# Kernel tuning notes

Measured on AMD Instinct MI355X. Metric: run time of the kernel, lower is better.

Reference implementation:

```python
import jax, jax.numpy as jnp
import numpy as np

MIN_NORM = 1e-15
BALL_EPS = 1e-3   # project() margin from ball boundary (c = 1)
TANH_CLIP = 15.0


def _norm(x):
    return jnp.sqrt(jnp.sum(x * x, axis=-1, keepdims=True)).clip(MIN_NORM)


def _tanh(x):
    return jnp.tanh(jnp.clip(x, -TANH_CLIP, TANH_CLIP))


def _artanh(x):
    return jnp.arctanh(jnp.clip(x, -1.0 + 1e-7, 1.0 - 1e-7))


def mobius_add(x, y):
    # Poincare ball Mobius addition, curvature c = 1
    x2 = jnp.sum(x * x, axis=-1, keepdims=True)
    y2 = jnp.sum(y * y, axis=-1, keepdims=True)
    xy = jnp.sum(x * y, axis=-1, keepdims=True)
    num = (1.0 + 2.0 * xy + y2) * x + (1.0 - x2) * y
    den = 1.0 + 2.0 * xy + x2 * y2
    return num / den.clip(MIN_NORM)


def project(x):
    norm = _norm(x)
    maxnorm = 1.0 - BALL_EPS
    return jnp.where(norm > maxnorm, x * (maxnorm / norm), x)


def expmap0(u):
    # exp map at the origin
    n = _norm(u)
    return _tanh(n) * u / n


def expmap(u, p):
    # exp map of tangent vector u at base point p
    n = _norm(u)
    p2 = jnp.sum(p * p, axis=-1, keepdims=True)
    lam = 2.0 / (1.0 - p2).clip(MIN_NORM)
    second = _tanh(0.5 * lam * n) * u / n
    return mobius_add(p, second)


def logmap(y, x):
    # log map of point y at base point x
    sub = mobius_add(-x, y)
    n = _norm(sub)
    x2 = jnp.sum(x * x, axis=-1, keepdims=True)
    lam = 2.0 / (1.0 - x2).clip(MIN_NORM)
    return (2.0 / lam) * _artanh(n) * sub / n


def setup_inputs() -> dict:
    key = jax.random.key(0)
    k1, k2, k3, k4 = jax.random.split(key, 4)
    n_entities, n_edges, n_rel, d = 100000, 800000, 32, 64
    # scale embeddings down so points stay well inside the unit ball
    ego_embed = 0.1 * jax.random.normal(k1, (n_entities, d), dtype=jnp.float32)
    relation_embed = 0.1 * jax.random.normal(k2, (n_rel, d), dtype=jnp.float32)
    edge_index = jax.random.randint(k3, (2, n_edges), 0, n_entities, dtype=jnp.int64)
    edge_type = jax.random.randint(k4, (n_edges,), 0, n_rel, dtype=jnp.int64)
    return {"ego_embed": ego_embed, "edge_index": edge_index,
            "edge_type": edge_type, "relation_embed": relation_embed}


def reference(ego_embed, edge_index, edge_type, relation_embed):
    head, tail = edge_index[0], edge_index[1]
    n_entities = ego_embed.shape[0]
    head_emb = ego_embed[head]          # [E, d] gather
    tail_emb = ego_embed[tail]          # [E, d] gather
    relation_emb = relation_embed[edge_type]  # [E, d] gather
    hyper_head = expmap0(head_emb)
    hyper_tail = expmap(tail_emb, hyper_head)
    hyper_rel = expmap(relation_emb, hyper_head)
    res = project(mobius_add(hyper_tail, hyper_rel))
    res = logmap(res, hyper_head)
    # scatter_mean over head index
    sums = jax.ops.segment_sum(res, head, num_segments=n_entities)
    counts = jax.ops.segment_sum(jnp.ones((head.shape[0],), dtype=res.dtype),
                                 head, num_segments=n_entities)
    entity_agg = sums / jnp.maximum(counts, 1.0)[:, None]
    return entity_agg
```

## Files before the change

### kernel.cpp

```cpp
#include <hip/hip_runtime.h>
#include <math.h>

#define D 64
#define MAXNORM 0.999f
#define MAXNORM2 (0.999f * 0.999f)
#define MIN_NORM 1e-15f
#define TANH_CLIP 15.0f
#define CAP 40

struct f4 { float x, y, z, w; };

__device__ __forceinline__ float frcp(float x) { return __builtin_amdgcn_rcpf(x); }
__device__ __forceinline__ float frsq(float x) { return __builtin_amdgcn_rsqf(x); }

__device__ __forceinline__ float dot8p(const f4& a0, const f4& a1,
                                       const f4& b0, const f4& b1) {
    return a0.x * b0.x + a0.y * b0.y + a0.z * b0.z + a0.w * b0.w +
           a1.x * b1.x + a1.y * b1.y + a1.z * b1.z + a1.w * b1.w;
}

__device__ __forceinline__ float rsum8(float v) {
    v += __shfl_xor(v, 1);
    v += __shfl_xor(v, 2);
    v += __shfl_xor(v, 4);
    return v;
}


__global__ void norm_kernel(const float* __restrict__ ego,
                            const float* __restrict__ rel,
                            float* __restrict__ norms,
                            float* __restrict__ relnorm,
                            float2* __restrict__ scal,
                            int N) {
    int wid = (blockIdx.x << 2) + (threadIdx.x >> 6);
    int lane = threadIdx.x & 63;
    if (wid >= N + 32) return;
    const float* src = (wid < N) ? (ego + (size_t)wid * D)
                                 : (rel + (size_t)(wid - N) * D);
    float v = src[lane];
    float s = v * v;
    s += __shfl_xor(s, 1);  s += __shfl_xor(s, 2);  s += __shfl_xor(s, 4);
    s += __shfl_xor(s, 8);  s += __shfl_xor(s, 16); s += __shfl_xor(s, 32);
    if (lane == 0) {
        float nh = sqrtf(s);
        if (wid < N) {
            norms[wid] = nh;
            float nhc = fmaxf(nh, MIN_NORM);
            float eh  = __expf(-2.0f * fminf(nhc, TANH_CLIP));
            float fp  = (1.0f - eh) * frcp((1.0f + eh) * nhc);
            float th2 = fp * fp * nhc * nhc;
            float tol = fmaxf(1.0f - th2, MIN_NORM);
            scal[wid] = make_float2(fp, tol);
        } else {
            relnorm[wid - N] = nh;
        }
    }
}


__global__ void bucket_kernel(const int* __restrict__ eidx,
                              const int* __restrict__ etype,
                              int* __restrict__ cnt,
                              int* __restrict__ bucket, int E) {
    int e = blockIdx.x * blockDim.x + threadIdx.x;
    if (e >= E) return;
    int head = eidx[e];
    int pos = atomicAdd(&cnt[head], 1);
    if (pos < CAP)
        bucket[head * CAP + pos] = eidx[E + e] | (etype[e] << 17);
}


__global__ void __launch_bounds__(256) agg_kernel(
        const float* __restrict__ ego,
        const float* __restrict__ rel,
        const int* __restrict__ cnt,
        const int* __restrict__ bucket,
        const float* __restrict__ norms,
        const float* __restrict__ relnorm,
        const float2* __restrict__ scal,
        float* __restrict__ out,
        int N) {
    int wid = (blockIdx.x * blockDim.x + threadIdx.x) >> 6;
    if (wid >= N) return;
    int lane = threadIdx.x & 63;
    int slot = lane >> 3;
    int sub  = lane & 7;

    int h = wid;
    const float* hrow = ego + (size_t)h * D;
    f4 h0 = *(const f4*)(hrow + sub * 4);
    f4 h1 = *(const f4*)(hrow + 32 + sub * 4);

    float2 sc2 = scal[h];
    float fp  = sc2.x;
    float tol = sc2.y;
    float p2  = 1.0f - tol;
    float hl  = frcp(tol);

    const int* brow = bucket + (size_t)h * CAP;
    int c = cnt[h];
    int cc = (c < CAP) ? c : CAP;
    f4 a0 = {0.f, 0.f, 0.f, 0.f}, a1 = {0.f, 0.f, 0.f, 0.f};
    float accP = 0.f;

    for (int i = slot; i < cc; i += 8) {
        int pk   = brow[i];
        int tail = pk & 0x1FFFF;
        int type = pk >> 17;

        const float* trow = ego + (size_t)tail * D;
        f4 t0 = *(const f4*)(trow + sub * 4);
        f4 t1 = *(const f4*)(trow + 32 + sub * 4);
        const float* rrow = rel + (size_t)type * D;
        f4 r0 = *(const f4*)(rrow + sub * 4);
        f4 r1 = *(const f4*)(rrow + 32 + sub * 4);
        float nt = norms[tail];
        float nr = relnorm[type];

        float d_ht = rsum8(dot8p(h0, h1, t0, t1));
        float d_hr = rsum8(dot8p(h0, h1, r0, r1));
        float d_tr = rsum8(dot8p(t0, t1, r0, r1));

        float t2 = nt * nt, r2 = nr * nr;
        float pt = fp * d_ht;
        float pr = fp * d_hr;

        float ntc = fmaxf(nt, MIN_NORM);
        float et  = __expf(-2.0f * fminf(hl * ntc, TANH_CLIP));
        float ft  = (1.0f - et) * frcp((1.0f + et) * ntc);
        float pyt = ft * pt;
        float yt2 = ft * ft * t2;
        float o1t = fmaf(2.0f, pyt, 1.0f);
        float at  = o1t + yt2;
        float invt = frcp(fmaf(p2, yt2, o1t));
        float At = at * invt;
        float Bt = tol * ft * invt;
        float x2 = (at - tol) * invt;

        float nrc = fmaxf(nr, MIN_NORM);
        float er  = __expf(-2.0f * fminf(hl * nrc, TANH_CLIP));
        float fr  = (1.0f - er) * frcp((1.0f + er) * nrc);
        float pyr = fr * pr;
        float gr  = fr * nr;
        float yr2 = gr * gr;
        float o1r = fmaf(2.0f, pyr, 1.0f);
        float ar  = o1r + yr2;
        float invr = frcp(fmaf(p2, yr2, o1r));
        float Ar = ar * invr;
        float Br = tol * fr * invr;
        float y2 = (ar - tol) * invr;

        float xy = At * Ar * p2 + At * Br * pr + Ar * Bt * pt + Bt * Br * d_tr;
        float o1m = fmaf(2.0f, xy, 1.0f);
        float am = o1m + y2;
        float bm = 1.0f - x2;
        float invm = frcp(fmaf(x2, y2, o1m));
        float al = (am * At + bm * Ar) * invm;
        float be = am * Bt * invm;
        float ga = bm * Br * invm;
        float m2 = fmaxf((am - bm) * invm, 1e-30f);

        if (m2 > MAXNORM2) {
            float s_ = MAXNORM * frsq(m2);
            al *= s_; be *= s_; ga *= s_;
            m2 = MAXNORM2;
        }

        float pm   = al * p2 + be * pt + ga * pr;
        float o2   = fmaf(-2.0f, pm, 1.0f);
        float invs = frcp(fmaf(p2, m2, o2));
        float om   = o2 + m2;
        float smm  = tol * invs;
        float u = fmaf(smm, al, -om * invs);
        float v = smm * be;
        float w = smm * ga;
        float s2 = fmaxf((om - tol) * invs, 1e-30f);

        float irs = frsq(s2);
        float ns  = fminf(s2 * irs, 1.0f - 1e-7f);
        float art = 0.5f * __logf((1.0f + ns) * frcp(1.0f - ns));
        float scv = tol * art * irs;

        float ct = scv * v, cr = scv * w;
        accP = fmaf(scv, u, accP);
        a0.x += ct * t0.x + cr * r0.x;  a0.y += ct * t0.y + cr * r0.y;
        a0.z += ct * t0.z + cr * r0.z;  a0.w += ct * t0.w + cr * r0.w;
        a1.x += ct * t1.x + cr * r1.x;  a1.y += ct * t1.y + cr * r1.y;
        a1.z += ct * t1.z + cr * r1.z;  a1.w += ct * t1.w + cr * r1.w;
    }

    #define RED(x) x += __shfl_xor(x, 8); x += __shfl_xor(x, 16); x += __shfl_xor(x, 32);
    RED(accP)
    RED(a0.x) RED(a0.y) RED(a0.z) RED(a0.w)
    RED(a1.x) RED(a1.y) RED(a1.z) RED(a1.w)
    #undef RED

    if (slot == 0) {
        float invc = frcp(fmaxf((float)c, 1.0f));
        float hp = accP * fp * invc;
        f4 o0, o1;
        o0.x = hp * h0.x + a0.x * invc;  o0.y = hp * h0.y + a0.y * invc;
        o0.z = hp * h0.z + a0.z * invc;  o0.w = hp * h0.w + a0.w * invc;
        o1.x = hp * h1.x + a1.x * invc;  o1.y = hp * h1.y + a1.y * invc;
        o1.z = hp * h1.z + a1.z * invc;  o1.w = hp * h1.w + a1.w * invc;
        float* orow = out + (size_t)h * D;
        *(f4*)(orow + sub * 4)      = o0;
        *(f4*)(orow + 32 + sub * 4) = o1;
    }
}

extern "C" void kernel_launch(void* const* d_in, const int* in_sizes, int n_in,
                              void* d_out, int out_size, void* d_ws, size_t ws_size,
                              hipStream_t stream) {
    const float* ego  = (const float*)d_in[0];
    const int*   eidx = (const int*)d_in[1];
    const int*   etyp = (const int*)d_in[2];
    const float* rel  = (const float*)d_in[3];
    float* out = (float*)d_out;

    int E = in_sizes[1] / 2;
    int N = in_sizes[0] / D;

    float2* scal  = (float2*)d_ws;
    int* cnt      = (int*)(scal + N);
    int* bucket   = cnt + N;
    float* norms   = (float*)(bucket + (size_t)N * CAP);
    float* relnorm = norms + N;

    hipMemsetAsync(cnt, 0, (size_t)N * sizeof(int), stream);

    const int tpb = 256;
    int eblocks = (E + tpb - 1) / tpb;
    int nblocks4 = (N + 32 + 3) / 4;

    norm_kernel<<<nblocks4, tpb, 0, stream>>>(ego, rel, norms, relnorm, scal, N);
    bucket_kernel<<<eblocks, tpb, 0, stream>>>(eidx, etyp, cnt, bucket, E);

    int nblocks = (N + 3) / 4;
    agg_kernel<<<nblocks, tpb, 0, stream>>>(ego, rel, cnt, bucket,
                                            norms, relnorm, scal, out, N);
}
```

Baseline: 158.4 us.

## Fuse norm and bucket kernels; widen edge parallelism to 16 slots per head

Merges the norm and bucket kernels into a single launch whose block range selects the role, removing one kernel launch and its serialization. In the aggregation kernel each wavefront now handles 16 edges at once with 4 lanes per edge, each lane owning 16 floats, instead of 8 edges with 8 lanes each. This halves the cross-lane shuffles needed for the dot products. The final reduction over slots now goes through shared memory instead of shuffles, so the kernel needs more registers for the accumulators and adds LDS traffic. Out-of-range wavefronts are clamped rather than exiting early so every thread reaches the shared-memory reduction.

```diff
diff --git a/kernel.cpp b/kernel.cpp
--- a/kernel.cpp
+++ b/kernel.cpp
@@ -13,27 +13,32 @@
 __device__ __forceinline__ float frcp(float x) { return __builtin_amdgcn_rcpf(x); }
 __device__ __forceinline__ float frsq(float x) { return __builtin_amdgcn_rsqf(x); }
 
-__device__ __forceinline__ float dot8p(const f4& a0, const f4& a1,
-                                       const f4& b0, const f4& b1) {
-    return a0.x * b0.x + a0.y * b0.y + a0.z * b0.z + a0.w * b0.w +
-           a1.x * b1.x + a1.y * b1.y + a1.z * b1.z + a1.w * b1.w;
-}
-
-__device__ __forceinline__ float rsum8(float v) {
-    v += __shfl_xor(v, 1);
-    v += __shfl_xor(v, 2);
-    v += __shfl_xor(v, 4);
-    return v;
-}
-
-
-__global__ void norm_kernel(const float* __restrict__ ego,
-                            const float* __restrict__ rel,
-                            float* __restrict__ norms,
-                            float* __restrict__ relnorm,
-                            float2* __restrict__ scal,
-                            int N) {
-    int wid = (blockIdx.x << 2) + (threadIdx.x >> 6);
+__device__ __forceinline__ float dot4(const f4& a, const f4& b) {
+    return a.x * b.x + a.y * b.y + a.z * b.z + a.w * b.w;
+}
+
+
+__global__ void setup_kernel(const float* __restrict__ ego,
+                             const float* __restrict__ rel,
+                             const int* __restrict__ eidx,
+                             const int* __restrict__ etype,
+                             int* __restrict__ cnt,
+                             int* __restrict__ bucket,
+                             float* __restrict__ norms,
+                             float* __restrict__ relnorm,
+                             float2* __restrict__ scal,
+                             int N, int E, int eblocks) {
+    if (blockIdx.x < eblocks) {
+        int e = blockIdx.x * 256 + threadIdx.x;
+        if (e < E) {
+            int head = eidx[e];
+            int pos = atomicAdd(&cnt[head], 1);
+            if (pos < CAP)
+                bucket[head * CAP + pos] = eidx[E + e] | (etype[e] << 17);
+        }
+        return;
+    }
+    int wid = (blockIdx.x - eblocks) * 4 + (threadIdx.x >> 6);
     int lane = threadIdx.x & 63;
     if (wid >= N + 32) return;
     const float* src = (wid < N) ? (ego + (size_t)wid * D)
@@ -59,19 +64,6 @@
 }
 
 
-__global__ void bucket_kernel(const int* __restrict__ eidx,
-                              const int* __restrict__ etype,
-                              int* __restrict__ cnt,
-                              int* __restrict__ bucket, int E) {
-    int e = blockIdx.x * blockDim.x + threadIdx.x;
-    if (e >= E) return;
-    int head = eidx[e];
-    int pos = atomicAdd(&cnt[head], 1);
-    if (pos < CAP)
-        bucket[head * CAP + pos] = eidx[E + e] | (etype[e] << 17);
-}
-
-
 __global__ void __launch_bounds__(256) agg_kernel(
         const float* __restrict__ ego,
         const float* __restrict__ rel,
@@ -82,16 +74,23 @@
         const float2* __restrict__ scal,
         float* __restrict__ out,
         int N) {
+    __shared__ float red[4][16][68];
+
     int wid = (blockIdx.x * blockDim.x + threadIdx.x) >> 6;
-    if (wid >= N) return;
+    int w    = threadIdx.x >> 6;
     int lane = threadIdx.x & 63;
-    int slot = lane >> 3;
-    int sub  = lane & 7;
-
-    int h = wid;
+    int slot = lane >> 2;
+    int sub  = lane & 3;
+
+    bool valid = (wid < N);
+    int h = valid ? wid : (N - 1);
+
     const float* hrow = ego + (size_t)h * D;
-    f4 h0 = *(const f4*)(hrow + sub * 4);
-    f4 h1 = *(const f4*)(hrow + 32 + sub * 4);
+    const float* hsub = hrow + sub * 16;
+    f4 h0 = *(const f4*)(hsub);
+    f4 h1 = *(const f4*)(hsub + 4);
+    f4 h2 = *(const f4*)(hsub + 8);
+    f4 h3 = *(const f4*)(hsub + 12);
 
     float2 sc2 = scal[h];
     float fp  = sc2.x;
@@ -102,28 +101,35 @@
     const int* brow = bucket + (size_t)h * CAP;
     int c = cnt[h];
     int cc = (c < CAP) ? c : CAP;
-    f4 a0 = {0.f, 0.f, 0.f, 0.f}, a1 = {0.f, 0.f, 0.f, 0.f};
+    f4 a0 = {0,0,0,0}, a1 = {0,0,0,0}, a2 = {0,0,0,0}, a3 = {0,0,0,0};
     float accP = 0.f;
 
-    for (int i = slot; i < cc; i += 8) {
+    for (int i = slot; i < cc; i += 16) {
         int pk   = brow[i];
         int tail = pk & 0x1FFFF;
         int type = pk >> 17;
 
-        const float* trow = ego + (size_t)tail * D;
-        f4 t0 = *(const f4*)(trow + sub * 4);
-        f4 t1 = *(const f4*)(trow + 32 + sub * 4);
-        const float* rrow = rel + (size_t)type * D;
-        f4 r0 = *(const f4*)(rrow + sub * 4);
-        f4 r1 = *(const f4*)(rrow + 32 + sub * 4);
+        const float* trow = ego + (size_t)tail * D + sub * 16;
+        f4 t0 = *(const f4*)(trow);
+        f4 t1 = *(const f4*)(trow + 4);
+        f4 t2 = *(const f4*)(trow + 8);
+        f4 t3 = *(const f4*)(trow + 12);
+        const float* rrow = rel + (size_t)type * D + sub * 16;
+        f4 r0 = *(const f4*)(rrow);
+        f4 r1 = *(const f4*)(rrow + 4);
+        f4 r2 = *(const f4*)(rrow + 8);
+        f4 r3 = *(const f4*)(rrow + 12);
         float nt = norms[tail];
         float nr = relnorm[type];
 
-        float d_ht = rsum8(dot8p(h0, h1, t0, t1));
-        float d_hr = rsum8(dot8p(h0, h1, r0, r1));
-        float d_tr = rsum8(dot8p(t0, t1, r0, r1));
-
-        float t2 = nt * nt, r2 = nr * nr;
+        float d_ht = dot4(h0,t0) + dot4(h1,t1) + dot4(h2,t2) + dot4(h3,t3);
+        float d_hr = dot4(h0,r0) + dot4(h1,r1) + dot4(h2,r2) + dot4(h3,r3);
+        float d_tr = dot4(t0,r0) + dot4(t1,r1) + dot4(t2,r2) + dot4(t3,r3);
+        d_ht += __shfl_xor(d_ht, 1); d_ht += __shfl_xor(d_ht, 2);
+        d_hr += __shfl_xor(d_hr, 1); d_hr += __shfl_xor(d_hr, 2);
+        d_tr += __shfl_xor(d_tr, 1); d_tr += __shfl_xor(d_tr, 2);
+
+        float t2n = nt * nt, r2n = nr * nr;
         float pt = fp * d_ht;
         float pr = fp * d_hr;
 
@@ -131,7 +137,7 @@
         float et  = __expf(-2.0f * fminf(hl * ntc, TANH_CLIP));
         float ft  = (1.0f - et) * frcp((1.0f + et) * ntc);
         float pyt = ft * pt;
-        float yt2 = ft * ft * t2;
+        float yt2 = ft * ft * t2n;
         float o1t = fmaf(2.0f, pyt, 1.0f);
         float at  = o1t + yt2;
         float invt = frcp(fmaf(p2, yt2, o1t));
@@ -175,7 +181,7 @@
         float smm  = tol * invs;
         float u = fmaf(smm, al, -om * invs);
         float v = smm * be;
-        float w = smm * ga;
+        float wv = smm * ga;
         float s2 = fmaxf((om - tol) * invs, 1e-30f);
 
         float irs = frsq(s2);
@@ -183,31 +189,43 @@
         float art = 0.5f * __logf((1.0f + ns) * frcp(1.0f - ns));
         float scv = tol * art * irs;
 
-        float ct = scv * v, cr = scv * w;
+        float ct = scv * v, cr = scv * wv;
         accP = fmaf(scv, u, accP);
-        a0.x += ct * t0.x + cr * r0.x;  a0.y += ct * t0.y + cr * r0.y;
-        a0.z += ct * t0.z + cr * r0.z;  a0.w += ct * t0.w + cr * r0.w;
-        a1.x += ct * t1.x + cr * r1.x;  a1.y += ct * t1.y + cr * r1.y;
-        a1.z += ct * t1.z + cr * r1.z;  a1.w += ct * t1.w + cr * r1.w;
-    }
-
-    #define RED(x) x += __shfl_xor(x, 8); x += __shfl_xor(x, 16); x += __shfl_xor(x, 32);
-    RED(accP)
-    RED(a0.x) RED(a0.y) RED(a0.z) RED(a0.w)
-    RED(a1.x) RED(a1.y) RED(a1.z) RED(a1.w)
-    #undef RED
-
-    if (slot == 0) {
+        a0.x = fmaf(ct, t0.x, fmaf(cr, r0.x, a0.x));
+        a0.y = fmaf(ct, t0.y, fmaf(cr, r0.y, a0.y));
+        a0.z = fmaf(ct, t0.z, fmaf(cr, r0.z, a0.z));
+        a0.w = fmaf(ct, t0.w, fmaf(cr, r0.w, a0.w));
+        a1.x = fmaf(ct, t1.x, fmaf(cr, r1.x, a1.x));
+        a1.y = fmaf(ct, t1.y, fmaf(cr, r1.y, a1.y));
+        a1.z = fmaf(ct, t1.z, fmaf(cr, r1.z, a1.z));
+        a1.w = fmaf(ct, t1.w, fmaf(cr, r1.w, a1.w));
+        a2.x = fmaf(ct, t2.x, fmaf(cr, r2.x, a2.x));
+        a2.y = fmaf(ct, t2.y, fmaf(cr, r2.y, a2.y));
+        a2.z = fmaf(ct, t2.z, fmaf(cr, r2.z, a2.z));
+        a2.w = fmaf(ct, t2.w, fmaf(cr, r2.w, a2.w));
+        a3.x = fmaf(ct, t3.x, fmaf(cr, r3.x, a3.x));
+        a3.y = fmaf(ct, t3.y, fmaf(cr, r3.y, a3.y));
+        a3.z = fmaf(ct, t3.z, fmaf(cr, r3.z, a3.z));
+        a3.w = fmaf(ct, t3.w, fmaf(cr, r3.w, a3.w));
+    }
+
+    accP += __shfl_xor(accP, 4);  accP += __shfl_xor(accP, 8);
+    accP += __shfl_xor(accP, 16); accP += __shfl_xor(accP, 32);
+
+    float* myrow = &red[w][slot][sub * 16];
+    *(f4*)(myrow)      = a0;
+    *(f4*)(myrow + 4)  = a1;
+    *(f4*)(myrow + 8)  = a2;
+    *(f4*)(myrow + 12) = a3;
+    float tot = 0.f;
+    #pragma unroll
+    for (int s = 0; s < 16; s++) tot += red[w][s][lane];
+
+    if (valid) {
         float invc = frcp(fmaxf((float)c, 1.0f));
         float hp = accP * fp * invc;
-        f4 o0, o1;
-        o0.x = hp * h0.x + a0.x * invc;  o0.y = hp * h0.y + a0.y * invc;
-        o0.z = hp * h0.z + a0.z * invc;  o0.w = hp * h0.w + a0.w * invc;
-        o1.x = hp * h1.x + a1.x * invc;  o1.y = hp * h1.y + a1.y * invc;
-        o1.z = hp * h1.z + a1.z * invc;  o1.w = hp * h1.w + a1.w * invc;
-        float* orow = out + (size_t)h * D;
-        *(f4*)(orow + sub * 4)      = o0;
-        *(f4*)(orow + 32 + sub * 4) = o1;
+        float hd = hrow[lane];
+        out[(size_t)h * D + lane] = fmaf(hp, hd, tot * invc);
     }
 }
 
@@ -233,10 +251,10 @@
 
     const int tpb = 256;
     int eblocks = (E + tpb - 1) / tpb;
-    int nblocks4 = (N + 32 + 3) / 4;
-
-    norm_kernel<<<nblocks4, tpb, 0, stream>>>(ego, rel, norms, relnorm, scal, N);
-    bucket_kernel<<<eblocks, tpb, 0, stream>>>(eidx, etyp, cnt, bucket, E);
+    int norm_blocks = (N + 32 + 3) / 4;
+
+    setup_kernel<<<eblocks + norm_blocks, tpb, 0, stream>>>(
+        ego, rel, eidx, etyp, cnt, bucket, norms, relnorm, scal, N, E, eblocks);
 
     int nblocks = (N + 3) / 4;
     agg_kernel<<<nblocks, tpb, 0, stream>>>(ego, rel, cnt, bucket,
```

Result: slower. 172.5 us (+8.9%).

## Sort heads by degree for aggregation and merge norm and bucket kernels

Applied to the files above, without the earlier changes.

Merges the norm and bucketing kernels into one launch, split by block index. Adds a degree histogram plus rank and order kernels that counting-sort heads by clamped degree, so each agg wavefront and block gets heads with similar edge counts. The aim is to cut loop-trip divergence and load imbalance in agg_kernel. In exchange it adds two kernel launches, hot atomics on a 41-bin histogram, and scattered head accesses and output writes.

```diff
diff --git a/kernel.cpp b/kernel.cpp
--- a/kernel.cpp
+++ b/kernel.cpp
@@ -7,6 +7,7 @@
 #define MIN_NORM 1e-15f
 #define TANH_CLIP 15.0f
 #define CAP 40
+#define NBIN 41
 
 struct f4 { float x, y, z, w; };
 
@@ -27,13 +28,27 @@
 }
 
 
-__global__ void norm_kernel(const float* __restrict__ ego,
-                            const float* __restrict__ rel,
-                            float* __restrict__ norms,
-                            float* __restrict__ relnorm,
-                            float2* __restrict__ scal,
-                            int N) {
-    int wid = (blockIdx.x << 2) + (threadIdx.x >> 6);
+__global__ void setup_kernel(const float* __restrict__ ego,
+                             const float* __restrict__ rel,
+                             const int* __restrict__ eidx,
+                             const int* __restrict__ etype,
+                             int* __restrict__ cnt,
+                             int* __restrict__ bucket,
+                             float* __restrict__ norms,
+                             float* __restrict__ relnorm,
+                             float2* __restrict__ scal,
+                             int N, int E, int eblocks) {
+    if (blockIdx.x < eblocks) {
+        int e = blockIdx.x * 256 + threadIdx.x;
+        if (e < E) {
+            int head = eidx[e];
+            int pos = atomicAdd(&cnt[head], 1);
+            if (pos < CAP)
+                bucket[head * CAP + pos] = eidx[E + e] | (etype[e] << 17);
+        }
+        return;
+    }
+    int wid = (blockIdx.x - eblocks) * 4 + (threadIdx.x >> 6);
     int lane = threadIdx.x & 63;
     if (wid >= N + 32) return;
     const float* src = (wid < N) ? (ego + (size_t)wid * D)
@@ -59,16 +74,31 @@
 }
 
 
-__global__ void bucket_kernel(const int* __restrict__ eidx,
-                              const int* __restrict__ etype,
-                              int* __restrict__ cnt,
-                              int* __restrict__ bucket, int E) {
-    int e = blockIdx.x * blockDim.x + threadIdx.x;
-    if (e >= E) return;
-    int head = eidx[e];
-    int pos = atomicAdd(&cnt[head], 1);
-    if (pos < CAP)
-        bucket[head * CAP + pos] = eidx[E + e] | (etype[e] << 17);
+__global__ void rank_kernel(const int* __restrict__ cnt,
+                            int* __restrict__ deghist,
+                            int* __restrict__ rankb, int N) {
+    int h = blockIdx.x * blockDim.x + threadIdx.x;
+    if (h >= N) return;
+    int d = cnt[h];
+    if (d > CAP) d = CAP;
+    rankb[h] = atomicAdd(&deghist[d], 1);
+}
+
+__global__ void order_kernel(const int* __restrict__ cnt,
+                             const int* __restrict__ deghist,
+                             const int* __restrict__ rankb,
+                             int* __restrict__ order, int N) {
+    __shared__ int binOff[NBIN];
+    if (threadIdx.x == 0) {
+        int run = 0;
+        for (int d = 0; d < NBIN; d++) { binOff[d] = run; run += deghist[d]; }
+    }
+    __syncthreads();
+    int h = blockIdx.x * blockDim.x + threadIdx.x;
+    if (h >= N) return;
+    int d = cnt[h];
+    if (d > CAP) d = CAP;
+    order[binOff[d] + rankb[h]] = h;
 }
 
 
@@ -80,6 +110,7 @@
         const float* __restrict__ norms,
         const float* __restrict__ relnorm,
         const float2* __restrict__ scal,
+        const int* __restrict__ order,
         float* __restrict__ out,
         int N) {
     int wid = (blockIdx.x * blockDim.x + threadIdx.x) >> 6;
@@ -88,7 +119,7 @@
     int slot = lane >> 3;
     int sub  = lane & 7;
 
-    int h = wid;
+    int h = order[wid];
     const float* hrow = ego + (size_t)h * D;
     f4 h0 = *(const f4*)(hrow + sub * 4);
     f4 h1 = *(const f4*)(hrow + 32 + sub * 4);
@@ -225,20 +256,26 @@
 
     float2* scal  = (float2*)d_ws;
     int* cnt      = (int*)(scal + N);
-    int* bucket   = cnt + N;
+    int* deghist  = cnt + N;
+    int* rankb    = deghist + 64;
+    int* order    = rankb + N;
+    int* bucket   = order + N;
     float* norms   = (float*)(bucket + (size_t)N * CAP);
     float* relnorm = norms + N;
 
-    hipMemsetAsync(cnt, 0, (size_t)N * sizeof(int), stream);
+    hipMemsetAsync(cnt, 0, (size_t)(N + 64) * sizeof(int), stream);
 
     const int tpb = 256;
     int eblocks = (E + tpb - 1) / tpb;
-    int nblocks4 = (N + 32 + 3) / 4;
-
-    norm_kernel<<<nblocks4, tpb, 0, stream>>>(ego, rel, norms, relnorm, scal, N);
-    bucket_kernel<<<eblocks, tpb, 0, stream>>>(eidx, etyp, cnt, bucket, E);
+    int norm_blocks = (N + 32 + 3) / 4;
+    int hblocks = (N + tpb - 1) / tpb;
+
+    setup_kernel<<<eblocks + norm_blocks, tpb, 0, stream>>>(
+        ego, rel, eidx, etyp, cnt, bucket, norms, relnorm, scal, N, E, eblocks);
+    rank_kernel<<<hblocks, tpb, 0, stream>>>(cnt, deghist, rankb, N);
+    order_kernel<<<hblocks, tpb, 0, stream>>>(cnt, deghist, rankb, order, N);
 
     int nblocks = (N + 3) / 4;
     agg_kernel<<<nblocks, tpb, 0, stream>>>(ego, rel, cnt, bucket,
-                                            norms, relnorm, scal, out, N);
-}
+                                            norms, relnorm, scal, order, out, N);
+}
```

New measurement: 498.8 us. 215% more time.
